# Kernel tuning notes

Hardware: AMD Instinct MI355X
Metric: run time of the kernel (lower is better)

## Reference

```python
import jax, jax.numpy as jnp
import numpy as np

M_DIM = 128   # vec_dim m
L_BAS = 64    # bas_dim L
RANK = 8      # sliding window length
BATCH = 32
SEQ = 2048


def _make_bbasis(L, m):
    # Bbasis[k, i] = cos(2*pi*(k+1)/(i+2)), fixed buffer
    k = jnp.arange(L, dtype=jnp.float32)[:, None]
    i = jnp.arange(m, dtype=jnp.float32)[None, :]
    return jnp.cos(2.0 * jnp.pi * (k + 1.0) / (i + 2.0))


def setup_inputs() -> dict:
    key = jax.random.key(0)
    k1, k2 = jax.random.split(key)
    seq_batch = jax.random.normal(k1, (BATCH, SEQ, M_DIM), dtype=jnp.float32)
    M = jnp.eye(M_DIM, dtype=jnp.float32)                     # nn.init.eye_
    Acoeff = jax.random.uniform(k2, (M_DIM, L_BAS), dtype=jnp.float32,
                                minval=-0.1, maxval=0.1)      # uniform(-0.1, 0.1)
    Bbasis = _make_bbasis(L_BAS, M_DIM)
    return {"seq_batch": seq_batch, "M": M, "Acoeff": Acoeff, "Bbasis": Bbasis}


def reference(seq_batch, M, Acoeff, Bbasis):
    B, S, m = seq_batch.shape
    L = Acoeff.shape[1]
    Nw = S - RANK + 1  # number of sliding windows (linear mode, stride 1)

    # unfold-equivalent: gather contiguous windows [B, Nw, RANK, m]
    idx = jnp.arange(Nw)[:, None] + jnp.arange(RANK)[None, :]
    windows = seq_batch[:, idx, :]
    agg = windows.mean(axis=2)              # rank_op='avg' -> [B, Nw, m]
    agg = jnp.einsum('bwm,nm->bwn', agg, M)  # agg @ M.T (linear map)

    # position-indexed basis target: N(k)[i] = Acoeff[i, k%L] * Bbasis[k%L, i]
    kmod = jnp.arange(Nw) % L
    Nk = Acoeff.T[kmod] * Bbasis[kmod]       # [Nw, m]

    # mean squared deviation over all windows / dims
    D = jnp.mean((agg - Nk[None, :, :]) ** 2)
    return D
```

## Files before the change

### kernel.cpp

```cpp
#include <hip/hip_runtime.h>

#define BATCH   32
#define SEQ     2048
#define MDIM    128
#define LBAS    64
#define NW      2041
#define TW      16
#define NTILE   8
#define APAD    136

typedef __attribute__((ext_vector_type(8))) short  short8;
typedef __attribute__((ext_vector_type(4))) float  float4v;

__device__ __forceinline__ unsigned short f2bf(float f) {
    unsigned int u = __float_as_uint(f);
    return (unsigned short)((u + 0x7FFFu + ((u >> 16) & 1u)) >> 16);
}
__device__ __forceinline__ void store_bf16x4(unsigned short* p, float4v a) {
    unsigned int lo = (unsigned)f2bf(a.x) | ((unsigned)f2bf(a.y) << 16);
    unsigned int hi = (unsigned)f2bf(a.z) | ((unsigned)f2bf(a.w) << 16);
    *reinterpret_cast<unsigned long long*>(p) = ((unsigned long long)hi << 32) | lo;
}

__global__ __launch_bounds__(256)
void ndd_prep(const float* __restrict__ Mmat,
              const float* __restrict__ Acoeff,
              const float* __restrict__ Bbasis,
              unsigned short* __restrict__ Mb,
              float* __restrict__ nk)
{
    const int gid = blockIdx.x * 256 + threadIdx.x;
    if (gid < 2048) {
        const int n = gid >> 4;
        const int c = gid & 15;
        const float* src = Mmat + n * MDIM + c * 8;
        short8 v;
        #pragma unroll
        for (int j = 0; j < 8; ++j) v[j] = (short)f2bf(src[j]);
        *reinterpret_cast<short8*>(Mb + ((size_t)(c * MDIM + n)) * 8) = v;
    } else if (gid < 2048 + 8192) {
        const int e = gid - 2048;
        const int k = e >> 7;
        const int n = e & 127;
        nk[k * MDIM + n] = Acoeff[n * LBAS + k] * Bbasis[k * MDIM + n];
    }
}

__global__ __launch_bounds__(256, 2)
void ndd_main(const float* __restrict__ x,
              const unsigned short* __restrict__ Mb,
              const float* __restrict__ nk,
              float* __restrict__ partial)
{
    __shared__ __align__(16) float sRaw[3][12 * 256];
    __shared__ __align__(16) unsigned short sA[TW * APAD];
    __shared__ float sred[4];

    const int tid  = threadIdx.x;
    const int lane = tid & 63;
    const int wave = tid >> 6;
    const int b    = blockIdx.x >> 4;
    const int base = (blockIdx.x & 15) * 128;
    const float* xb = x + (size_t)b * SEQ * MDIM;

    const int l15 = lane & 15;
    const int q   = lane >> 4;
    const int nb  = wave * 32;

    short8 bfr[4][2];
    #pragma unroll
    for (int kk = 0; kk < 4; ++kk)
        #pragma unroll
        for (int nj = 0; nj < 2; ++nj)
            bfr[kk][nj] = *reinterpret_cast<const short8*>(
                Mb + ((size_t)((kk * 4 + q) * MDIM + nb + nj * 16 + l15)) * 8);

    float nkreg[4][2][4];
    #pragma unroll
    for (int p = 0; p < 4; ++p)
        #pragma unroll
        for (int nj = 0; nj < 2; ++nj)
            #pragma unroll
            for (int r = 0; r < 4; ++r)
                nkreg[p][nj][r] = nk[(p * 16 + q * 4 + r) * MDIM + nb + nj * 16 + l15];

    auto issue = [&](int j) {
        const int W0r = base + j * TW;
        #pragma unroll
        for (int i = 0; i < 3; ++i) {
            const int c = wave * 3 + i;
            int r0 = W0r + 2 * c;
            r0 = r0 > 2046 ? 2046 : r0;
            const float* g = xb + (size_t)r0 * MDIM + lane * 4;
            __builtin_amdgcn_global_load_lds(
                (const __attribute__((address_space(1))) void*)g,
                (__attribute__((address_space(3))) void*)&sRaw[j % 3][c * 256],
                16, 0, 0);
        }
    };
    issue(0);
    issue(1);

    float local = 0.f;

    #pragma unroll
    for (int j = 0; j < NTILE; ++j) {
        __builtin_amdgcn_sched_barrier(0);
        if (j == NTILE - 1) __builtin_amdgcn_s_waitcnt(0x0F70);
        else                __builtin_amdgcn_s_waitcnt(0x0F73);
        asm volatile("s_barrier" ::: "memory");
        __builtin_amdgcn_sched_barrier(0);

        {
            const int m4 = tid & 31;
            const int wg = tid >> 5;
            const float4v* R = reinterpret_cast<const float4v*>(&sRaw[j % 3][0]);
            float4v rows[9];
            #pragma unroll
            for (int i = 0; i < 9; ++i) rows[i] = R[(wg * 2 + i) * 32 + m4];
            float4v acc = ((rows[0] + rows[1]) + (rows[2] + rows[3])) +
                          ((rows[4] + rows[5]) + (rows[6] + rows[7]));
            store_bf16x4(&sA[(wg * 2) * APAD + m4 * 4], acc * 0.125f);
            acc += rows[8] - rows[0];
            store_bf16x4(&sA[(wg * 2 + 1) * APAD + m4 * 4], acc * 0.125f);
        }

        __builtin_amdgcn_sched_barrier(0);
        __builtin_amdgcn_s_waitcnt(0xC07F);
        asm volatile("s_barrier" ::: "memory");
        __builtin_amdgcn_sched_barrier(0);

        if (j + 2 < NTILE) issue(j + 2);

        float4v accf[2] = {(float4v){0.f,0.f,0.f,0.f}, (float4v){0.f,0.f,0.f,0.f}};
        #pragma unroll
        for (int kk = 0; kk < 4; ++kk) {
            const short8 af = *reinterpret_cast<const short8*>(
                &sA[l15 * APAD + kk * 32 + q * 8]);
            #pragma unroll
            for (int nj = 0; nj < 2; ++nj)
                accf[nj] = __builtin_amdgcn_mfma_f32_16x16x32_bf16(
                    af, bfr[kk][nj], accf[nj], 0, 0, 0);
        }

        const int p = j & 3;
        #pragma unroll
        for (int nj = 0; nj < 2; ++nj) {
            #pragma unroll
            for (int r = 0; r < 4; ++r) {
                const int w = base + j * TW + q * 4 + r;
                if (w < NW) {
                    const float d = accf[nj][r] - nkreg[p][nj][r];
                    local += d * d;
                }
            }
        }
    }

    #pragma unroll
    for (int off = 32; off > 0; off >>= 1)
        local += __shfl_down(local, off, 64);
    if (lane == 0) sred[wave] = local;
    __syncthreads();
    if (tid == 0)
        partial[blockIdx.x] = (sred[0] + sred[1]) + (sred[2] + sred[3]);
}

__global__ __launch_bounds__(256)
void ndd_reduce(const float* __restrict__ partial, float* __restrict__ out)
{
    __shared__ float sred[4];
    float s = partial[threadIdx.x] + partial[threadIdx.x + 256];
    #pragma unroll
    for (int off = 32; off > 0; off >>= 1) s += __shfl_down(s, off, 64);
    if ((threadIdx.x & 63) == 0) sred[threadIdx.x >> 6] = s;
    __syncthreads();
    if (threadIdx.x == 0)
        out[0] = ((sred[0] + sred[1]) + (sred[2] + sred[3])) * (1.0f / 8359936.0f);
}

extern "C" void kernel_launch(void* const* d_in, const int* in_sizes, int n_in,
                              void* d_out, int out_size, void* d_ws, size_t ws_size,
                              hipStream_t stream) {
    const float* x     = (const float*)d_in[0];
    const float* Mmat  = (const float*)d_in[1];
    const float* Acoef = (const float*)d_in[2];
    const float* Bbas  = (const float*)d_in[3];
    float* out         = (float*)d_out;

    unsigned short* Mb = (unsigned short*)d_ws;
    float* nkp         = (float*)((char*)d_ws + 32768);
    float* part        = (float*)((char*)d_ws + 65536);

    ndd_prep<<<40, 256, 0, stream>>>(Mmat, Acoef, Bbas, Mb, nkp);
    ndd_main<<<512, 256, 0, stream>>>(x, Mb, nkp, part);
    ndd_reduce<<<1, 256, 0, stream>>>(part, out);
}
```

Before: 83.30 us.

## Fuse prep and reduce into main kernel, deepen load pipeline to four buffers

Removes the separate prep kernel: each block now converts its M fragments to bf16 and computes its Nk target values directly from Acoeff and Bbasis. The final reduction kernel is replaced by an atomicAdd into a memset output. The LDS ring for raw input rows grows from three to four buffers so three tiles are in flight, with matching waitcnt thresholds. This trades two kernel launches for redundant per-block prep work, more LDS per block, and a nondeterministic atomic summation order.

```diff
diff --git a/kernel.cpp b/kernel.cpp
--- a/kernel.cpp
+++ b/kernel.cpp
@@ -7,6 +7,7 @@
 #define NW      2041
 #define TW      16
 #define NTILE   8
+#define NBUF    4
 #define APAD    136
 
 typedef __attribute__((ext_vector_type(8))) short  short8;
@@ -21,38 +22,21 @@
     unsigned int hi = (unsigned)f2bf(a.z) | ((unsigned)f2bf(a.w) << 16);
     *reinterpret_cast<unsigned long long*>(p) = ((unsigned long long)hi << 32) | lo;
 }
-
-__global__ __launch_bounds__(256)
-void ndd_prep(const float* __restrict__ Mmat,
-              const float* __restrict__ Acoeff,
-              const float* __restrict__ Bbasis,
-              unsigned short* __restrict__ Mb,
-              float* __restrict__ nk)
-{
-    const int gid = blockIdx.x * 256 + threadIdx.x;
-    if (gid < 2048) {
-        const int n = gid >> 4;
-        const int c = gid & 15;
-        const float* src = Mmat + n * MDIM + c * 8;
-        short8 v;
-        #pragma unroll
-        for (int j = 0; j < 8; ++j) v[j] = (short)f2bf(src[j]);
-        *reinterpret_cast<short8*>(Mb + ((size_t)(c * MDIM + n)) * 8) = v;
-    } else if (gid < 2048 + 8192) {
-        const int e = gid - 2048;
-        const int k = e >> 7;
-        const int n = e & 127;
-        nk[k * MDIM + n] = Acoeff[n * LBAS + k] * Bbasis[k * MDIM + n];
-    }
+__device__ __forceinline__ short8 pack_bf16x8(float4v a, float4v b) {
+    short8 r;
+    r[0]=(short)f2bf(a.x); r[1]=(short)f2bf(a.y); r[2]=(short)f2bf(a.z); r[3]=(short)f2bf(a.w);
+    r[4]=(short)f2bf(b.x); r[5]=(short)f2bf(b.y); r[6]=(short)f2bf(b.z); r[7]=(short)f2bf(b.w);
+    return r;
 }
 
 __global__ __launch_bounds__(256, 2)
-void ndd_main(const float* __restrict__ x,
-              const unsigned short* __restrict__ Mb,
-              const float* __restrict__ nk,
-              float* __restrict__ partial)
+void ndd_fused(const float* __restrict__ x,
+               const float* __restrict__ Mmat,
+               const float* __restrict__ Acoeff,
+               const float* __restrict__ Bbasis,
+               float* __restrict__ out)
 {
-    __shared__ __align__(16) float sRaw[3][12 * 256];
+    __shared__ __align__(16) float sRaw[NBUF][12 * 256];
     __shared__ __align__(16) unsigned short sA[TW * APAD];
     __shared__ float sred[4];
 
@@ -67,23 +51,6 @@
     const int q   = lane >> 4;
     const int nb  = wave * 32;
 
-    short8 bfr[4][2];
-    #pragma unroll
-    for (int kk = 0; kk < 4; ++kk)
-        #pragma unroll
-        for (int nj = 0; nj < 2; ++nj)
-            bfr[kk][nj] = *reinterpret_cast<const short8*>(
-                Mb + ((size_t)((kk * 4 + q) * MDIM + nb + nj * 16 + l15)) * 8);
-
-    float nkreg[4][2][4];
-    #pragma unroll
-    for (int p = 0; p < 4; ++p)
-        #pragma unroll
-        for (int nj = 0; nj < 2; ++nj)
-            #pragma unroll
-            for (int r = 0; r < 4; ++r)
-                nkreg[p][nj][r] = nk[(p * 16 + q * 4 + r) * MDIM + nb + nj * 16 + l15];
-
     auto issue = [&](int j) {
         const int W0r = base + j * TW;
         #pragma unroll
@@ -94,27 +61,52 @@
             const float* g = xb + (size_t)r0 * MDIM + lane * 4;
             __builtin_amdgcn_global_load_lds(
                 (const __attribute__((address_space(1))) void*)g,
-                (__attribute__((address_space(3))) void*)&sRaw[j % 3][c * 256],
+                (__attribute__((address_space(3))) void*)&sRaw[j & 3][c * 256],
                 16, 0, 0);
         }
     };
-    issue(0);
-    issue(1);
+    issue(0); issue(1); issue(2);
+
+    short8 bfr[4][2];
+    #pragma unroll
+    for (int kk = 0; kk < 4; ++kk)
+        #pragma unroll
+        for (int nj = 0; nj < 2; ++nj) {
+            const float* src = Mmat + (size_t)(nb + nj * 16 + l15) * MDIM + kk * 32 + q * 8;
+            float4v lo = *reinterpret_cast<const float4v*>(src);
+            float4v hi = *reinterpret_cast<const float4v*>(src + 4);
+            bfr[kk][nj] = pack_bf16x8(lo, hi);
+        }
+
+    float nkreg[4][2][4];
+    #pragma unroll
+    for (int nj = 0; nj < 2; ++nj) {
+        const int n = nb + nj * 16 + l15;
+        #pragma unroll
+        for (int p = 0; p < 4; ++p) {
+            float4v ac = *reinterpret_cast<const float4v*>(
+                Acoeff + (size_t)n * LBAS + p * 16 + q * 4);
+            #pragma unroll
+            for (int r = 0; r < 4; ++r)
+                nkreg[p][nj][r] = ac[r] * Bbasis[(p * 16 + q * 4 + r) * MDIM + n];
+        }
+    }
 
     float local = 0.f;
 
     #pragma unroll
     for (int j = 0; j < NTILE; ++j) {
         __builtin_amdgcn_sched_barrier(0);
-        if (j == NTILE - 1) __builtin_amdgcn_s_waitcnt(0x0F70);
-        else                __builtin_amdgcn_s_waitcnt(0x0F73);
+        if (j <= NTILE - 3)      __builtin_amdgcn_s_waitcnt(0x0F76);
+        else if (j == NTILE - 2) __builtin_amdgcn_s_waitcnt(0x0F73);
+        else                     __builtin_amdgcn_s_waitcnt(0x0F70);
         asm volatile("s_barrier" ::: "memory");
         __builtin_amdgcn_sched_barrier(0);
 
         {
             const int m4 = tid & 31;
             const int wg = tid >> 5;
-            const float4v* R = reinterpret_cast<const float4v*>(&sRaw[j % 3][0]);
+            const float4v* R = reinterpret_cast<const float4v*>(&sRaw[j & 3][0]);
             float4v rows[9];
             #pragma unroll
             for (int i = 0; i < 9; ++i) rows[i] = R[(wg * 2 + i) * 32 + m4];
@@ -130,7 +122,7 @@
         asm volatile("s_barrier" ::: "memory");
         __builtin_amdgcn_sched_barrier(0);
 
-        if (j + 2 < NTILE) issue(j + 2);
+        if (j + 3 < NTILE) issue(j + 3);
 
         float4v accf[2] = {(float4v){0.f,0.f,0.f,0.f}, (float4v){0.f,0.f,0.f,0.f}};
         #pragma unroll
@@ -163,20 +155,8 @@
     if (lane == 0) sred[wave] = local;
     __syncthreads();
     if (tid == 0)
-        partial[blockIdx.x] = (sred[0] + sred[1]) + (sred[2] + sred[3]);
-}
-
-__global__ __launch_bounds__(256)
-void ndd_reduce(const float* __restrict__ partial, float* __restrict__ out)
-{
-    __shared__ float sred[4];
-    float s = partial[threadIdx.x] + partial[threadIdx.x + 256];
-    #pragma unroll
-    for (int off = 32; off > 0; off >>= 1) s += __shfl_down(s, off, 64);
-    if ((threadIdx.x & 63) == 0) sred[threadIdx.x >> 6] = s;
-    __syncthreads();
-    if (threadIdx.x == 0)
-        out[0] = ((sred[0] + sred[1]) + (sred[2] + sred[3])) * (1.0f / 8359936.0f);
+        atomicAdd(out, ((sred[0] + sred[1]) + (sred[2] + sred[3]))
+                           * (1.0f / 8359936.0f));
 }
 
 extern "C" void kernel_launch(void* const* d_in, const int* in_sizes, int n_in,
@@ -188,11 +168,6 @@
     const float* Bbas  = (const float*)d_in[3];
     float* out         = (float*)d_out;
 
-    unsigned short* Mb = (unsigned short*)d_ws;
-    float* nkp         = (float*)((char*)d_ws + 32768);
-    float* part        = (float*)((char*)d_ws + 65536);
-
-    ndd_prep<<<40, 256, 0, stream>>>(Mmat, Acoef, Bbas, Mb, nkp);
-    ndd_main<<<512, 256, 0, stream>>>(x, Mb, nkp, part);
-    ndd_reduce<<<1, 256, 0, stream>>>(part, out);
+    hipMemsetAsync(out, 0, sizeof(float), stream);
+    ndd_fused<<<512, 256, 0, stream>>>(x, Mmat, Acoef, Bbas, out);
 }
```

Result: slower. 89.87 us (+7.9%).

## Double window tile size, double-buffer raw rows, and slide running sum over eight windows

Applied to the files above, without the earlier changes.

Each loop step now covers 32 windows instead of 16, so a block runs half as many tiles and half as many barrier pairs. The raw-row staging drops from a triple buffer to a double buffer, which changes the wait counts. The window average becomes a running sum that slides across 8 consecutive windows per thread, using 128 threads instead of all 256, which cuts redundant row additions. The 1/8 scale is folded into the bf16 M matrix in the prep kernel. The trade-offs are larger per-tile loads, a shallower prefetch depth, and half the threads sitting idle during the averaging phase.

```diff
diff --git a/kernel.cpp b/kernel.cpp
--- a/kernel.cpp
+++ b/kernel.cpp
@@ -5,8 +5,8 @@
 #define MDIM    128
 #define LBAS    64
 #define NW      2041
-#define TW      16
-#define NTILE   8
+#define TW      32
+#define NTILE   4
 #define APAD    136
 
 typedef __attribute__((ext_vector_type(8))) short  short8;
@@ -36,7 +36,7 @@
         const float* src = Mmat + n * MDIM + c * 8;
         short8 v;
         #pragma unroll
-        for (int j = 0; j < 8; ++j) v[j] = (short)f2bf(src[j]);
+        for (int j = 0; j < 8; ++j) v[j] = (short)f2bf(src[j] * 0.125f);
         *reinterpret_cast<short8*>(Mb + ((size_t)(c * MDIM + n)) * 8) = v;
     } else if (gid < 2048 + 8192) {
         const int e = gid - 2048;
@@ -52,7 +52,7 @@
               const float* __restrict__ nk,
               float* __restrict__ partial)
 {
-    __shared__ __align__(16) float sRaw[3][12 * 256];
+    __shared__ __align__(16) float sRaw[2][20 * 256];
     __shared__ __align__(16) unsigned short sA[TW * APAD];
     __shared__ float sred[4];
 
@@ -75,26 +75,29 @@
             bfr[kk][nj] = *reinterpret_cast<const short8*>(
                 Mb + ((size_t)((kk * 4 + q) * MDIM + nb + nj * 16 + l15)) * 8);
 
-    float nkreg[4][2][4];
-    #pragma unroll
-    for (int p = 0; p < 4; ++p)
-        #pragma unroll
-        for (int nj = 0; nj < 2; ++nj)
-            #pragma unroll
-            for (int r = 0; r < 4; ++r)
-                nkreg[p][nj][r] = nk[(p * 16 + q * 4 + r) * MDIM + nb + nj * 16 + l15];
+    float nkreg[2][2][2][4];
+    #pragma unroll
+    for (int p = 0; p < 2; ++p)
+        #pragma unroll
+        for (int wi = 0; wi < 2; ++wi)
+            #pragma unroll
+            for (int nj = 0; nj < 2; ++nj)
+                #pragma unroll
+                for (int r = 0; r < 4; ++r)
+                    nkreg[p][wi][nj][r] =
+                        nk[(p * 32 + wi * 16 + q * 4 + r) * MDIM + nb + nj * 16 + l15];
 
     auto issue = [&](int j) {
         const int W0r = base + j * TW;
         #pragma unroll
-        for (int i = 0; i < 3; ++i) {
-            const int c = wave * 3 + i;
+        for (int i = 0; i < 5; ++i) {
+            const int c = wave * 5 + i;
             int r0 = W0r + 2 * c;
             r0 = r0 > 2046 ? 2046 : r0;
             const float* g = xb + (size_t)r0 * MDIM + lane * 4;
             __builtin_amdgcn_global_load_lds(
                 (const __attribute__((address_space(1))) void*)g,
-                (__attribute__((address_space(3))) void*)&sRaw[j % 3][c * 256],
+                (__attribute__((address_space(3))) void*)&sRaw[j & 1][c * 256],
                 16, 0, 0);
         }
     };
@@ -107,22 +110,26 @@
     for (int j = 0; j < NTILE; ++j) {
         __builtin_amdgcn_sched_barrier(0);
         if (j == NTILE - 1) __builtin_amdgcn_s_waitcnt(0x0F70);
-        else                __builtin_amdgcn_s_waitcnt(0x0F73);
+        else                __builtin_amdgcn_s_waitcnt(0x0F75);
         asm volatile("s_barrier" ::: "memory");
         __builtin_amdgcn_sched_barrier(0);
 
-        {
-            const int m4 = tid & 31;
-            const int wg = tid >> 5;
-            const float4v* R = reinterpret_cast<const float4v*>(&sRaw[j % 3][0]);
-            float4v rows[9];
-            #pragma unroll
-            for (int i = 0; i < 9; ++i) rows[i] = R[(wg * 2 + i) * 32 + m4];
+        if (tid < 128) {
+            const int m4  = tid & 31;
+            const int seg = tid >> 5;
+            const float4v* R = reinterpret_cast<const float4v*>(&sRaw[j & 1][0]);
+            float4v rows[15];
+            #pragma unroll
+            for (int i = 0; i < 15; ++i)
+                rows[i] = R[(seg * 8 + i) * 32 + m4];
             float4v acc = ((rows[0] + rows[1]) + (rows[2] + rows[3])) +
                           ((rows[4] + rows[5]) + (rows[6] + rows[7]));
-            store_bf16x4(&sA[(wg * 2) * APAD + m4 * 4], acc * 0.125f);
-            acc += rows[8] - rows[0];
-            store_bf16x4(&sA[(wg * 2 + 1) * APAD + m4 * 4], acc * 0.125f);
+            store_bf16x4(&sA[(seg * 8) * APAD + m4 * 4], acc);
+            #pragma unroll
+            for (int t = 1; t < 8; ++t) {
+                acc += rows[7 + t] - rows[t - 1];
+                store_bf16x4(&sA[(seg * 8 + t) * APAD + m4 * 4], acc);
+            }
         }
 
         __builtin_amdgcn_sched_barrier(0);
@@ -132,26 +139,39 @@
 
         if (j + 2 < NTILE) issue(j + 2);
 
-        float4v accf[2] = {(float4v){0.f,0.f,0.f,0.f}, (float4v){0.f,0.f,0.f,0.f}};
+        float4v accf[2][2];
+        #pragma unroll
+        for (int wi = 0; wi < 2; ++wi)
+            #pragma unroll
+            for (int nj = 0; nj < 2; ++nj)
+                accf[wi][nj] = (float4v){0.f, 0.f, 0.f, 0.f};
         #pragma unroll
         for (int kk = 0; kk < 4; ++kk) {
-            const short8 af = *reinterpret_cast<const short8*>(
-                &sA[l15 * APAD + kk * 32 + q * 8]);
-            #pragma unroll
-            for (int nj = 0; nj < 2; ++nj)
-                accf[nj] = __builtin_amdgcn_mfma_f32_16x16x32_bf16(
-                    af, bfr[kk][nj], accf[nj], 0, 0, 0);
-        }
-
-        const int p = j & 3;
-        #pragma unroll
-        for (int nj = 0; nj < 2; ++nj) {
-            #pragma unroll
-            for (int r = 0; r < 4; ++r) {
-                const int w = base + j * TW + q * 4 + r;
-                if (w < NW) {
-                    const float d = accf[nj][r] - nkreg[p][nj][r];
-                    local += d * d;
+            short8 af[2];
+            #pragma unroll
+            for (int wi = 0; wi < 2; ++wi)
+                af[wi] = *reinterpret_cast<const short8*>(
+                    &sA[(wi * 16 + l15) * APAD + kk * 32 + q * 8]);
+            #pragma unroll
+            for (int wi = 0; wi < 2; ++wi)
+                #pragma unroll
+                for (int nj = 0; nj < 2; ++nj)
+                    accf[wi][nj] = __builtin_amdgcn_mfma_f32_16x16x32_bf16(
+                        af[wi], bfr[kk][nj], accf[wi][nj], 0, 0, 0);
+        }
+
+        const int p = j & 1;
+        #pragma unroll
+        for (int wi = 0; wi < 2; ++wi) {
+            #pragma unroll
+            for (int nj = 0; nj < 2; ++nj) {
+                #pragma unroll
+                for (int r = 0; r < 4; ++r) {
+                    const int w = base + j * TW + wi * 16 + q * 4 + r;
+                    if (w < NW) {
+                        const float d = accf[wi][nj][r] - nkreg[p][wi][nj][r];
+                        local += d * d;
+                    }
                 }
             }
         }
```

Result: no change. 84.49 us (+1.4%).
